# Performance work log

Measured on AMD Instinct MI355X. Metric: run time of the kernel, lower is better.

## Reference

```python
import jax, jax.numpy as jnp
import numpy as np

C = 256
GROUPS = 32
EPS = 1e-5


def setup_inputs() -> dict:
    key = jax.random.key(0)
    ks = jax.random.split(key, 6)
    b, c, H, W = 8, C, 64, 64
    s = 1.0 / np.sqrt(c)
    return {
        "x": jax.random.normal(ks[0], (b, c, H, W), dtype=jnp.float32),
        "gn_scale": jnp.ones((c,), jnp.float32),
        "gn_bias": jnp.zeros((c,), jnp.float32),
        "wq": jax.random.normal(ks[1], (c, c), jnp.float32) * s,
        "bq": jnp.zeros((c,), jnp.float32),
        "wk": jax.random.normal(ks[2], (c, c), jnp.float32) * s,
        "bk": jnp.zeros((c,), jnp.float32),
        "wv": jax.random.normal(ks[3], (c, c), jnp.float32) * s,
        "bv": jnp.zeros((c,), jnp.float32),
        "wo": jax.random.normal(ks[4], (c, c), jnp.float32) * s,
        "bo": jnp.zeros((c,), jnp.float32),
    }


def reference(x, gn_scale, gn_bias, wq, bq, wk, bk, wv, bv, wo, bo):
    b, c, H, W = x.shape
    N = H * W
    # GroupNorm(32, c)
    xg = x.reshape(b, GROUPS, c // GROUPS, H, W)
    mean = xg.mean(axis=(2, 3, 4), keepdims=True)
    var = xg.var(axis=(2, 3, 4), keepdims=True)
    xn = ((xg - mean) * jax.lax.rsqrt(var + EPS)).reshape(b, c, H, W)
    xn = xn * gn_scale[None, :, None, None] + gn_bias[None, :, None, None]
    xf = xn.reshape(b, c, N)  # [b, c, N]
    # 1x1 convs == per-pixel channel matmuls
    q = jnp.einsum('oc,bcn->bon', wq, xf) + bq[None, :, None]
    k = jnp.einsum('oc,bcn->bon', wk, xf) + bk[None, :, None]
    v = jnp.einsum('oc,bcn->bon', wv, xf) + bv[None, :, None]
    # attention: scores [b, N, N]
    scale = 1.0 / jnp.sqrt(jnp.asarray(c, x.dtype))
    w = jnp.einsum('bcn,bcm->bnm', q, k) * scale
    w = jax.nn.softmax(w, axis=-1)
    attn = jnp.einsum('bnm,bcm->bcn', w, v)  # [b, c, N]
    out = jnp.einsum('oc,bcn->bon', wo, attn) + bo[None, :, None]
    return x + out.reshape(b, c, H, W)
```

## Files before the change

kernel.cpp:

```cpp
#include <hip/hip_runtime.h>

typedef __attribute__((ext_vector_type(8))) short short8;
typedef __attribute__((ext_vector_type(4))) float floatx4;
typedef __attribute__((ext_vector_type(16))) float floatx16;
typedef __attribute__((ext_vector_type(4))) int intx4;

#define NPIX 4096
#define CH 256

static __device__ __forceinline__ unsigned short f2bf(float f) {
  union { float f; unsigned int u; } v; v.f = f;
  unsigned int u = v.u;
  return (unsigned short)((u + 0x7FFFu + ((u >> 16) & 1u)) >> 16);
}

static __device__ __forceinline__ unsigned int pk2bf(float a, float b) {
  union { float f; unsigned int u; } x, y; x.f = a; y.f = b;
  return __builtin_amdgcn_perm(y.u + 0x8000u, x.u + 0x8000u, 0x07060302u);
}

typedef __attribute__((address_space(3))) unsigned int lds_uint;
typedef const __attribute__((address_space(1))) unsigned int glob_uint;
static __device__ __forceinline__ void gload16(const void* g, void* l) {
  __builtin_amdgcn_global_load_lds((glob_uint*)g, (lds_uint*)l, 16, 0, 0);
}

__global__ void conv_weights_kernel(const float* __restrict__ wq, const float* __restrict__ wk,
                                    const float* __restrict__ wv, const float* __restrict__ wo,
                                    unsigned short* __restrict__ wqkv, unsigned short* __restrict__ wob) {
  int i = blockIdx.x * 256 + threadIdx.x;
  wqkv[i]          = f2bf(wq[i]);
  wqkv[65536 + i]  = f2bf(wk[i]);
  wqkv[131072 + i] = f2bf(wv[i]);
  wob[i]           = f2bf(wo[i]);
}

__global__ __launch_bounds__(256) void gn_kernel(const float* __restrict__ x,
                                                 const float* __restrict__ gsc,
                                                 const float* __restrict__ gbi,
                                                 unsigned short* __restrict__ xnT) {
  int blk = blockIdx.x; int b = blk >> 5; int g = blk & 31;
  int c0 = g * 8;
  const float* xb = x + ((size_t)b * CH + c0) * NPIX;
  int tid = threadIdx.x;
  float s = 0.f, ss = 0.f;
#pragma unroll
  for (int ci = 0; ci < 8; ++ci) {
    const floatx4* p = (const floatx4*)(xb + (size_t)ci * NPIX);
    for (int n4 = tid; n4 < 1024; n4 += 256) {
      floatx4 v = p[n4];
      s += v[0] + v[1] + v[2] + v[3];
      ss += v[0]*v[0] + v[1]*v[1] + v[2]*v[2] + v[3]*v[3];
    }
  }
#pragma unroll
  for (int o = 32; o > 0; o >>= 1) { s += __shfl_down(s, o); ss += __shfl_down(ss, o); }
  __shared__ float red[10];
  int wid = tid >> 6;
  if ((tid & 63) == 0) { red[wid] = s; red[4 + wid] = ss; }
  __syncthreads();
  if (tid == 0) {
    float S = red[0] + red[1] + red[2] + red[3];
    float SS = red[4] + red[5] + red[6] + red[7];
    float mean = S * (1.f / 32768.f);
    float var = SS * (1.f / 32768.f) - mean * mean;
    red[8] = mean; red[9] = rsqrtf(var + 1e-5f);
  }
  __syncthreads();
  float mean = red[8], rstd = red[9];
  float sc[8], bi[8];
#pragma unroll
  for (int ci = 0; ci < 8; ++ci) {
    float scale = gsc[c0 + ci] * rstd;
    sc[ci] = scale;
    bi[ci] = gbi[c0 + ci] - mean * scale;
  }
  for (int n4 = tid; n4 < 1024; n4 += 256) {
    floatx4 v[8];
#pragma unroll
    for (int ci = 0; ci < 8; ++ci) v[ci] = ((const floatx4*)(xb + (size_t)ci * NPIX))[n4];
#pragma unroll
    for (int j = 0; j < 4; ++j) {
      alignas(16) unsigned short tmp[8];
#pragma unroll
      for (int ci = 0; ci < 8; ++ci) tmp[ci] = f2bf(v[ci][j] * sc[ci] + bi[ci]);
      *(intx4*)(xnT + ((size_t)(b * NPIX + n4 * 4 + j)) * CH + c0) = *(const intx4*)tmp;
    }
  }
}

__global__ __launch_bounds__(256, 2) void qkv_gemm(
    const unsigned short* __restrict__ wqkv, const unsigned short* __restrict__ xnT,
    const float* __restrict__ bq, const float* __restrict__ bk, const float* __restrict__ bv,
    unsigned short* __restrict__ qT, unsigned short* __restrict__ kT, unsigned short* __restrict__ vC) {
  int nt = blockIdx.x, ot = blockIdx.y, bz = blockIdx.z;
  int which = bz % 3, b = bz / 3;
  const unsigned short* W = wqkv + which * 65536;
  const float* bias = which == 0 ? bq : (which == 1 ? bk : bv);
  const unsigned short* X = xnT + (size_t)b * NPIX * CH;
  int o0 = ot * 128, n0 = nt * 128;

  __shared__ unsigned short As[128 * 64];
  __shared__ unsigned short Bs[128 * 64];

  int tid = threadIdx.x;
  int wave = tid >> 6, lane = tid & 63, quad = lane >> 4, l16 = lane & 15;
  int wm = (wave >> 1) * 64, wn = (wave & 1) * 64;

  floatx4 acc[4][4];
#pragma unroll
  for (int i = 0; i < 4; ++i)
#pragma unroll
    for (int j = 0; j < 4; ++j) acc[i][j] = (floatx4){0.f, 0.f, 0.f, 0.f};

  for (int k0 = 0; k0 < 256; k0 += 64) {
    __syncthreads();
#pragma unroll
    for (int c2 = 0; c2 < 4; ++c2) {
      int row = wave * 32 + c2 * 8 + (lane >> 3);
      int sc = (lane & 7) ^ (row & 7);
      gload16(W + (size_t)(o0 + row) * CH + k0 + sc * 8, &As[(wave * 32 + c2 * 8) * 64]);
      gload16(X + (size_t)(n0 + row) * CH + k0 + sc * 8, &Bs[(wave * 32 + c2 * 8) * 64]);
    }
    __syncthreads();
#pragma unroll
    for (int s = 0; s < 2; ++s) {
      short8 af[4], bf[4];
#pragma unroll
      for (int i = 0; i < 4; ++i) {
        int m = wm + i * 16 + l16;
        af[i] = *(const short8*)(As + m * 64 + (((s * 4 + quad) ^ (m & 7)) * 8));
        int n = wn + i * 16 + l16;
        bf[i] = *(const short8*)(Bs + n * 64 + (((s * 4 + quad) ^ (n & 7)) * 8));
      }
#pragma unroll
      for (int i = 0; i < 4; ++i)
#pragma unroll
        for (int j = 0; j < 4; ++j)
          acc[i][j] = __builtin_amdgcn_mfma_f32_16x16x32_bf16(af[i], bf[j], acc[i][j], 0, 0, 0);
    }
  }

  if (which < 2) {
    float qs = (which == 0) ? 0.090168440f : 1.0f;
    unsigned short* outp = (which == 0 ? qT : kT) + (size_t)b * NPIX * CH;
#pragma unroll
    for (int i = 0; i < 4; ++i) {
      int obase = o0 + wm + i * 16 + quad * 4;
      float bias4[4];
#pragma unroll
      for (int r = 0; r < 4; ++r) bias4[r] = bias[obase + r];
#pragma unroll
      for (int j = 0; j < 4; ++j) {
        int n = n0 + wn + j * 16 + l16;
        uint2 pk;
        pk.x = pk2bf((acc[i][j][0] + bias4[0]) * qs, (acc[i][j][1] + bias4[1]) * qs);
        pk.y = pk2bf((acc[i][j][2] + bias4[2]) * qs, (acc[i][j][3] + bias4[3]) * qs);
        *(uint2*)(outp + (size_t)n * CH + obase) = pk;
      }
    }
  } else {
    unsigned short* outp = vC + (size_t)b * CH * NPIX;
#pragma unroll
    for (int i = 0; i < 4; ++i)
#pragma unroll
      for (int r = 0; r < 4; ++r) {
        int o = o0 + wm + i * 16 + quad * 4 + r;
        float bb = bias[o];
#pragma unroll
        for (int j = 0; j < 4; ++j) {
          int n = n0 + wn + j * 16 + l16;
          outp[(size_t)o * NPIX + n] = f2bf(acc[i][j][r] + bb);
        }
      }
  }
}

__global__ __launch_bounds__(512, 2) void attn_kernel(
    const unsigned short* __restrict__ qT, const unsigned short* __restrict__ kT,
    const unsigned short* __restrict__ vC, unsigned short* __restrict__ aT) {
  __shared__ unsigned short Klds[2][64 * 256];
  __shared__ unsigned short Vlds[2][256 * 64];
  __shared__ unsigned short Plds[128 * 64];
  __shared__ float lred[128][2];

  const int tid = threadIdx.x;
  const int w = tid >> 6, lane = tid & 63;
  const int l32 = lane & 31, h = lane >> 5;
  const int b = blockIdx.x & 7, qt = blockIdx.x >> 3;
  const int qbase = qt * 128;

  const unsigned short* Kb = kT + (size_t)b * NPIX * CH;
  const unsigned short* Vb = vC + (size_t)b * CH * NPIX;

  const int msl = (w & 1) * 32, qsl = (w >> 1) * 32;
  const int csl = (w & 3) * 64, qh = (w >> 2) * 64;

  short8 qf[16];
  {
    const unsigned short* qp = qT + ((size_t)(b * NPIX + qbase + qsl + l32)) * CH + h * 8;
#pragma unroll
    for (int s = 0; s < 16; ++s) qf[s] = *(const short8*)(qp + s * 16);
  }

  floatx16 oacc[2][2] = {};
  float l_acc = 0.f;

#define STAGE(KT)                                                                         \
  {                                                                                       \
    int m0_ = (KT) * 64;                                                                  \
    int bb_ = (KT) & 1;                                                                   \
    if (w < 4) {                                                                          \
      _Pragma("unroll") for (int j = 0; j < 8; ++j) {                                     \
        int r0 = w * 16 + j * 2 + (lane >> 5);                                            \
        gload16(Kb + (size_t)(m0_ + r0) * CH + (((lane & 31) ^ (r0 & 7)) * 8),            \
                &Klds[bb_][(w * 16 + j * 2) * 256]);                                      \
      }                                                                                   \
    } else {                                                                              \
      _Pragma("unroll") for (int j = 0; j < 8; ++j) {                                     \
        int c_ = (w - 4) * 64 + j * 8 + (lane >> 3);                                      \
        gload16(Vb + (size_t)c_ * NPIX + m0_ + (((lane & 7) ^ (c_ & 7)) * 8),             \
                &Vlds[bb_][((w - 4) * 64 + j * 8) * 64]);                                 \
      }                                                                                   \
    }                                                                                     \
  }

  STAGE(0);

  for (int kt = 0; kt < 64; ++kt) {
    const int buf = kt & 1;
    asm volatile("s_waitcnt vmcnt(0) lgkmcnt(0)\ns_barrier" ::: "memory");
    if (kt + 1 < 64) STAGE(kt + 1);

    floatx16 sacc = {};
    {
      const int m = msl + l32;
      const unsigned short* kr = &Klds[buf][m * 256];
      const int mx = m & 7;
#pragma unroll
      for (int s = 0; s < 16; ++s) {
        short8 kf = *(const short8*)(kr + (((s * 2 + h) ^ mx) * 8));
        sacc = __builtin_amdgcn_mfma_f32_32x32x16_bf16(kf, qf[s], sacc, 0, 0, 0);
      }
    }
    float sum = 0.f;
#pragma unroll
    for (int r = 0; r < 16; ++r) {
      float p = exp2f(sacc[r]);
      sacc[r] = p; sum += p;
    }
    sum += __shfl_xor(sum, 32);
    l_acc += sum;

    {
      int qrow = qsl + l32;
#pragma unroll
      for (int t = 0; t < 4; ++t) {
        int phys = ((msl >> 3) + t) ^ (qrow & 7);
        uint2 wv;
        wv.x = pk2bf(sacc[4 * t], sacc[4 * t + 1]);
        wv.y = pk2bf(sacc[4 * t + 2], sacc[4 * t + 3]);
        *(uint2*)&Plds[qrow * 64 + phys * 8 + h * 4] = wv;
      }
    }
    asm volatile("s_waitcnt lgkmcnt(0)\ns_barrier" ::: "memory");

#pragma unroll
    for (int mstep = 0; mstep < 4; ++mstep) {
      short8 pf[2], vf[2];
#pragma unroll
      for (int qsub = 0; qsub < 2; ++qsub) {
        int q = qh + qsub * 32 + l32;
        pf[qsub] = *(const short8*)&Plds[q * 64 + (((mstep * 2 + h) ^ (q & 7)) * 8)];
      }
#pragma unroll
      for (int csub = 0; csub < 2; ++csub) {
        int c = csl + csub * 32 + l32;
        vf[csub] = *(const short8*)&Vlds[buf][c * 64 + (((mstep * 2 + h) ^ (c & 7)) * 8)];
      }
#pragma unroll
      for (int csub = 0; csub < 2; ++csub)
#pragma unroll
        for (int qsub = 0; qsub < 2; ++qsub)
          oacc[csub][qsub] =
              __builtin_amdgcn_mfma_f32_32x32x16_bf16(vf[csub], pf[qsub], oacc[csub][qsub], 0, 0, 0);
    }
  }
#undef STAGE

  if (lane < 32) lred[qsl + l32][w & 1] = l_acc;
  __syncthreads();
  float inv[2];
#pragma unroll
  for (int qsub = 0; qsub < 2; ++qsub) {
    int q = qh + qsub * 32 + l32;
    inv[qsub] = 1.f / (lred[q][0] + lred[q][1]);
  }
  unsigned short* ab = aT + (size_t)b * NPIX * CH;
#pragma unroll
  for (int csub = 0; csub < 2; ++csub)
#pragma unroll
    for (int qsub = 0; qsub < 2; ++qsub) {
      int qg = qbase + qh + qsub * 32 + l32;
      float iv = inv[qsub];
#pragma unroll
      for (int t = 0; t < 4; ++t) {
        int c = csl + csub * 32 + 8 * t + 4 * h;
        uint2 wv;
        wv.x = pk2bf(oacc[csub][qsub][4 * t] * iv, oacc[csub][qsub][4 * t + 1] * iv);
        wv.y = pk2bf(oacc[csub][qsub][4 * t + 2] * iv, oacc[csub][qsub][4 * t + 3] * iv);
        *(uint2*)(ab + (size_t)qg * CH + c) = wv;
      }
    }
}

__global__ __launch_bounds__(256, 2) void out_gemm(
    const unsigned short* __restrict__ wob, const unsigned short* __restrict__ aT,
    const float* __restrict__ bo, const float* __restrict__ x, float* __restrict__ outp) {
  int nt = blockIdx.x, ot = blockIdx.y, b = blockIdx.z;
  const unsigned short* A = aT + (size_t)b * NPIX * CH;
  int o0 = ot * 128, n0 = nt * 128;

  __shared__ unsigned short As[128 * 64];
  __shared__ unsigned short Bs[128 * 64];

  int tid = threadIdx.x;
  int wave = tid >> 6, lane = tid & 63, quad = lane >> 4, l16 = lane & 15;
  int wm = (wave >> 1) * 64, wn = (wave & 1) * 64;

  floatx4 acc[4][4];
#pragma unroll
  for (int i = 0; i < 4; ++i)
#pragma unroll
    for (int j = 0; j < 4; ++j) acc[i][j] = (floatx4){0.f, 0.f, 0.f, 0.f};

  for (int k0 = 0; k0 < 256; k0 += 64) {
    __syncthreads();
#pragma unroll
    for (int c2 = 0; c2 < 4; ++c2) {
      int row = wave * 32 + c2 * 8 + (lane >> 3);
      int sc = (lane & 7) ^ (row & 7);
      gload16(wob + (size_t)(o0 + row) * CH + k0 + sc * 8, &As[(wave * 32 + c2 * 8) * 64]);
      gload16(A + (size_t)(n0 + row) * CH + k0 + sc * 8, &Bs[(wave * 32 + c2 * 8) * 64]);
    }
    __syncthreads();
#pragma unroll
    for (int s = 0; s < 2; ++s) {
      short8 af[4], bf[4];
#pragma unroll
      for (int i = 0; i < 4; ++i) {
        int m = wm + i * 16 + l16;
        af[i] = *(const short8*)(As + m * 64 + (((s * 4 + quad) ^ (m & 7)) * 8));
        int n = wn + i * 16 + l16;
        bf[i] = *(const short8*)(Bs + n * 64 + (((s * 4 + quad) ^ (n & 7)) * 8));
      }
#pragma unroll
      for (int i = 0; i < 4; ++i)
#pragma unroll
        for (int j = 0; j < 4; ++j)
          acc[i][j] = __builtin_amdgcn_mfma_f32_16x16x32_bf16(af[i], bf[j], acc[i][j], 0, 0, 0);
    }
  }

#pragma unroll
  for (int i = 0; i < 4; ++i)
#pragma unroll
    for (int r = 0; r < 4; ++r) {
      int o = o0 + wm + i * 16 + quad * 4 + r;
      float bb = bo[o];
#pragma unroll
      for (int j = 0; j < 4; ++j) {
        int n = n0 + wn + j * 16 + l16;
        size_t idx = ((size_t)b * CH + o) * NPIX + n;
        outp[idx] = x[idx] + bb + acc[i][j][r];
      }
    }
}

extern "C" void kernel_launch(void* const* d_in, const int* in_sizes, int n_in,
                              void* d_out, int out_size, void* d_ws, size_t ws_size,
                              hipStream_t stream) {
  const float* x   = (const float*)d_in[0];
  const float* gsc = (const float*)d_in[1];
  const float* gbi = (const float*)d_in[2];
  const float* wq  = (const float*)d_in[3];
  const float* bq  = (const float*)d_in[4];
  const float* wk  = (const float*)d_in[5];
  const float* bk  = (const float*)d_in[6];
  const float* wv  = (const float*)d_in[7];
  const float* bv  = (const float*)d_in[8];
  const float* wo  = (const float*)d_in[9];
  const float* bo  = (const float*)d_in[10];
  float* out = (float*)d_out;

  char* ws = (char*)d_ws;
  unsigned short* xnT  = (unsigned short*)(ws);
  unsigned short* qT   = (unsigned short*)(ws + 16777216);
  unsigned short* kT   = (unsigned short*)(ws + 33554432);
  unsigned short* vC   = (unsigned short*)(ws + 50331648);
  unsigned short* wqkv = (unsigned short*)(ws + 67108864);
  unsigned short* wob  = (unsigned short*)(ws + 67502080);
  unsigned short* aT   = (unsigned short*)(ws + 67633152);

  conv_weights_kernel<<<256, 256, 0, stream>>>(wq, wk, wv, wo, wqkv, wob);
  gn_kernel<<<256, 256, 0, stream>>>(x, gsc, gbi, xnT);
  dim3 g1(32, 2, 24);
  qkv_gemm<<<g1, 256, 0, stream>>>(wqkv, xnT, bq, bk, bv, qT, kT, vC);
  attn_kernel<<<256, 512, 0, stream>>>(qT, kT, vC, aT);
  dim3 g3(32, 2, 8);
  out_gemm<<<g3, 256, 0, stream>>>(wob, aT, bo, x, out);
}
```

Baseline: 320.9 us.

## Warp-specialize attention into score and PV waves; cache GroupNorm input in LDS

The attention kernel is split by role. Four waves compute QK^T scores and exp into double-buffered P tiles. The other four waves issue the K/V global-to-LDS loads and run the PV MFMAs one step behind, so score and output work overlap. The KV tile shrinks from 64 to 32 rows, which cuts LDS use (possibly allowing two blocks per CU) but doubles the number of barriers. Separately, the GroupNorm kernel keeps the group's input in 128KB of LDS so the normalization pass does not read x from global memory a second time, at the cost of occupancy for that kernel.

```diff
diff --git a/kernel.cpp b/kernel.cpp
--- a/kernel.cpp
+++ b/kernel.cpp
@@ -39,6 +39,8 @@
                                                  const float* __restrict__ gsc,
                                                  const float* __restrict__ gbi,
                                                  unsigned short* __restrict__ xnT) {
+  __shared__ float xs[8 * 4096];
+  __shared__ float red[12];
   int blk = blockIdx.x; int b = blk >> 5; int g = blk & 31;
   int c0 = g * 8;
   const float* xb = x + ((size_t)b * CH + c0) * NPIX;
@@ -47,15 +49,16 @@
 #pragma unroll
   for (int ci = 0; ci < 8; ++ci) {
     const floatx4* p = (const floatx4*)(xb + (size_t)ci * NPIX);
+    floatx4* ls = (floatx4*)(xs + ci * 4096);
     for (int n4 = tid; n4 < 1024; n4 += 256) {
       floatx4 v = p[n4];
+      ls[n4] = v;
       s += v[0] + v[1] + v[2] + v[3];
       ss += v[0]*v[0] + v[1]*v[1] + v[2]*v[2] + v[3]*v[3];
     }
   }
 #pragma unroll
   for (int o = 32; o > 0; o >>= 1) { s += __shfl_down(s, o); ss += __shfl_down(ss, o); }
-  __shared__ float red[10];
   int wid = tid >> 6;
   if ((tid & 63) == 0) { red[wid] = s; red[4 + wid] = ss; }
   __syncthreads();
@@ -78,7 +81,7 @@
   for (int n4 = tid; n4 < 1024; n4 += 256) {
     floatx4 v[8];
 #pragma unroll
-    for (int ci = 0; ci < 8; ++ci) v[ci] = ((const floatx4*)(xb + (size_t)ci * NPIX))[n4];
+    for (int ci = 0; ci < 8; ++ci) v[ci] = ((const floatx4*)(xs + ci * 4096))[n4];
 #pragma unroll
     for (int j = 0; j < 4; ++j) {
       alignas(16) unsigned short tmp[8];
@@ -179,10 +182,10 @@
 __global__ __launch_bounds__(512, 2) void attn_kernel(
     const unsigned short* __restrict__ qT, const unsigned short* __restrict__ kT,
     const unsigned short* __restrict__ vC, unsigned short* __restrict__ aT) {
-  __shared__ unsigned short Klds[2][64 * 256];
-  __shared__ unsigned short Vlds[2][256 * 64];
-  __shared__ unsigned short Plds[128 * 64];
-  __shared__ float lred[128][2];
+  __shared__ unsigned short Klds[2][32 * 256];
+  __shared__ unsigned short Vlds[2][256 * 32];
+  __shared__ unsigned short Plds[2][128 * 32];
+  __shared__ float lred[128];
 
   const int tid = threadIdx.x;
   const int w = tid >> 6, lane = tid & 63;
@@ -193,125 +196,133 @@
   const unsigned short* Kb = kT + (size_t)b * NPIX * CH;
   const unsigned short* Vb = vC + (size_t)b * CH * NPIX;
 
-  const int msl = (w & 1) * 32, qsl = (w >> 1) * 32;
-  const int csl = (w & 3) * 64, qh = (w >> 2) * 64;
-
-  short8 qf[16];
-  {
-    const unsigned short* qp = qT + ((size_t)(b * NPIX + qbase + qsl + l32)) * CH + h * 8;
-#pragma unroll
-    for (int s = 0; s < 16; ++s) qf[s] = *(const short8*)(qp + s * 16);
-  }
-
-  floatx16 oacc[2][2] = {};
-  float l_acc = 0.f;
-
-#define STAGE(KT)                                                                         \
-  {                                                                                       \
-    int m0_ = (KT) * 64;                                                                  \
-    int bb_ = (KT) & 1;                                                                   \
-    if (w < 4) {                                                                          \
-      _Pragma("unroll") for (int j = 0; j < 8; ++j) {                                     \
-        int r0 = w * 16 + j * 2 + (lane >> 5);                                            \
-        gload16(Kb + (size_t)(m0_ + r0) * CH + (((lane & 31) ^ (r0 & 7)) * 8),            \
-                &Klds[bb_][(w * 16 + j * 2) * 256]);                                      \
-      }                                                                                   \
-    } else {                                                                              \
-      _Pragma("unroll") for (int j = 0; j < 8; ++j) {                                     \
-        int c_ = (w - 4) * 64 + j * 8 + (lane >> 3);                                      \
-        gload16(Vb + (size_t)c_ * NPIX + m0_ + (((lane & 7) ^ (c_ & 7)) * 8),             \
-                &Vlds[bb_][((w - 4) * 64 + j * 8) * 64]);                                 \
-      }                                                                                   \
-    }                                                                                     \
-  }
-
-  STAGE(0);
-
-  for (int kt = 0; kt < 64; ++kt) {
-    const int buf = kt & 1;
-    asm volatile("s_waitcnt vmcnt(0) lgkmcnt(0)\ns_barrier" ::: "memory");
-    if (kt + 1 < 64) STAGE(kt + 1);
-
-    floatx16 sacc = {};
+#define BARRIER() asm volatile("s_waitcnt vmcnt(0) lgkmcnt(0)\ns_barrier" ::: "memory")
+
+  if (w < 4) {
+    const int qsl = w * 32;
+    const int q = qsl + l32;
+    const int swq = (q >> 1) & 3;
+    const int mx = l32 & 7;
+    short8 qf[16];
     {
-      const int m = msl + l32;
-      const unsigned short* kr = &Klds[buf][m * 256];
-      const int mx = m & 7;
-#pragma unroll
-      for (int s = 0; s < 16; ++s) {
-        short8 kf = *(const short8*)(kr + (((s * 2 + h) ^ mx) * 8));
-        sacc = __builtin_amdgcn_mfma_f32_32x32x16_bf16(kf, qf[s], sacc, 0, 0, 0);
-      }
-    }
-    float sum = 0.f;
-#pragma unroll
-    for (int r = 0; r < 16; ++r) {
-      float p = exp2f(sacc[r]);
-      sacc[r] = p; sum += p;
-    }
-    sum += __shfl_xor(sum, 32);
-    l_acc += sum;
-
-    {
-      int qrow = qsl + l32;
-#pragma unroll
-      for (int t = 0; t < 4; ++t) {
-        int phys = ((msl >> 3) + t) ^ (qrow & 7);
-        uint2 wv;
-        wv.x = pk2bf(sacc[4 * t], sacc[4 * t + 1]);
-        wv.y = pk2bf(sacc[4 * t + 2], sacc[4 * t + 3]);
-        *(uint2*)&Plds[qrow * 64 + phys * 8 + h * 4] = wv;
-      }
-    }
-    asm volatile("s_waitcnt lgkmcnt(0)\ns_barrier" ::: "memory");
-
-#pragma unroll
-    for (int mstep = 0; mstep < 4; ++mstep) {
-      short8 pf[2], vf[2];
-#pragma unroll
-      for (int qsub = 0; qsub < 2; ++qsub) {
-        int q = qh + qsub * 32 + l32;
-        pf[qsub] = *(const short8*)&Plds[q * 64 + (((mstep * 2 + h) ^ (q & 7)) * 8)];
-      }
-#pragma unroll
-      for (int csub = 0; csub < 2; ++csub) {
-        int c = csl + csub * 32 + l32;
-        vf[csub] = *(const short8*)&Vlds[buf][c * 64 + (((mstep * 2 + h) ^ (c & 7)) * 8)];
-      }
-#pragma unroll
-      for (int csub = 0; csub < 2; ++csub)
-#pragma unroll
-        for (int qsub = 0; qsub < 2; ++qsub)
-          oacc[csub][qsub] =
-              __builtin_amdgcn_mfma_f32_32x32x16_bf16(vf[csub], pf[qsub], oacc[csub][qsub], 0, 0, 0);
-    }
-  }
-#undef STAGE
-
-  if (lane < 32) lred[qsl + l32][w & 1] = l_acc;
-  __syncthreads();
-  float inv[2];
-#pragma unroll
-  for (int qsub = 0; qsub < 2; ++qsub) {
-    int q = qh + qsub * 32 + l32;
-    inv[qsub] = 1.f / (lred[q][0] + lred[q][1]);
-  }
-  unsigned short* ab = aT + (size_t)b * NPIX * CH;
-#pragma unroll
-  for (int csub = 0; csub < 2; ++csub)
-#pragma unroll
-    for (int qsub = 0; qsub < 2; ++qsub) {
-      int qg = qbase + qh + qsub * 32 + l32;
-      float iv = inv[qsub];
-#pragma unroll
-      for (int t = 0; t < 4; ++t) {
-        int c = csl + csub * 32 + 8 * t + 4 * h;
-        uint2 wv;
-        wv.x = pk2bf(oacc[csub][qsub][4 * t] * iv, oacc[csub][qsub][4 * t + 1] * iv);
-        wv.y = pk2bf(oacc[csub][qsub][4 * t + 2] * iv, oacc[csub][qsub][4 * t + 3] * iv);
-        *(uint2*)(ab + (size_t)qg * CH + c) = wv;
-      }
-    }
+      const unsigned short* qp = qT + ((size_t)(b * NPIX + qbase + q)) * CH + h * 8;
+#pragma unroll
+      for (int s = 0; s < 16; ++s) qf[s] = *(const short8*)(qp + s * 16);
+    }
+    float l_acc = 0.f;
+    for (int t = 0; t < 129; ++t) {
+      BARRIER();
+      if (t < 128) {
+        const unsigned short* kr = &Klds[t & 1][l32 * 256];
+        floatx16 s0 = {}, s1 = {};
+#pragma unroll
+        for (int s = 0; s < 8; ++s) {
+          short8 kf0 = *(const short8*)(kr + (((s * 2 + h) ^ mx) * 8));
+          short8 kf1 = *(const short8*)(kr + ((((s + 8) * 2 + h) ^ mx) * 8));
+          s0 = __builtin_amdgcn_mfma_f32_32x32x16_bf16(kf0, qf[s], s0, 0, 0, 0);
+          s1 = __builtin_amdgcn_mfma_f32_32x32x16_bf16(kf1, qf[s + 8], s1, 0, 0, 0);
+        }
+        float sum = 0.f;
+#pragma unroll
+        for (int r = 0; r < 16; ++r) {
+          float pv = exp2f(s0[r] + s1[r]);
+          s0[r] = pv; sum += pv;
+        }
+        l_acc += sum;
+        unsigned short* Pw = Plds[t & 1];
+#pragma unroll
+        for (int t4 = 0; t4 < 4; ++t4) {
+          int phys = t4 ^ swq;
+          uint2 wv;
+          wv.x = pk2bf(s0[4 * t4], s0[4 * t4 + 1]);
+          wv.y = pk2bf(s0[4 * t4 + 2], s0[4 * t4 + 3]);
+          *(uint2*)&Pw[q * 32 + phys * 8 + h * 4] = wv;
+        }
+      }
+    }
+    l_acc += __shfl_xor(l_acc, 32);
+    if (lane < 32) lred[q] = l_acc;
+    BARRIER();
+  } else {
+    const int p = w - 4;
+    const int csl = p * 64;
+    floatx16 oacc[2][4];
+#pragma unroll
+    for (int i = 0; i < 2; ++i)
+#pragma unroll
+      for (int j = 0; j < 4; ++j) oacc[i][j] = (floatx16){0.f};
+#pragma unroll
+    for (int j = 0; j < 4; ++j) {
+      int r0 = p * 8 + j * 2 + h;
+      gload16(Kb + (size_t)r0 * CH + (((lane & 31) ^ (r0 & 7)) * 8),
+              &Klds[0][(p * 8 + j * 2) * 256]);
+    }
+    for (int t = 0; t < 129; ++t) {
+      BARRIER();
+      if (t < 128) {
+        const int m0 = t * 32;
+#pragma unroll
+        for (int j = 0; j < 4; ++j) {
+          int r = p * 64 + j * 16 + (lane >> 2);
+          gload16(Vb + (size_t)r * NPIX + m0 + (((lane & 3) ^ ((r >> 1) & 3)) * 8),
+                  &Vlds[t & 1][(p * 64 + j * 16) * 32]);
+        }
+        if (t + 1 < 128) {
+          const int m1 = (t + 1) * 32;
+#pragma unroll
+          for (int j = 0; j < 4; ++j) {
+            int r0 = p * 8 + j * 2 + h;
+            gload16(Kb + (size_t)(m1 + r0) * CH + (((lane & 31) ^ (r0 & 7)) * 8),
+                    &Klds[(t + 1) & 1][(p * 8 + j * 2) * 256]);
+          }
+        }
+      }
+      if (t >= 1) {
+        const int pb = (t - 1) & 1;
+#pragma unroll
+        for (int mstep = 0; mstep < 2; ++mstep) {
+          short8 pf[4], vf[2];
+#pragma unroll
+          for (int qs = 0; qs < 4; ++qs) {
+            int q = qs * 32 + l32;
+            pf[qs] = *(const short8*)&Plds[pb][q * 32 + (((mstep * 2 + h) ^ ((q >> 1) & 3)) * 8)];
+          }
+#pragma unroll
+          for (int cs = 0; cs < 2; ++cs) {
+            int c = csl + cs * 32 + l32;
+            vf[cs] = *(const short8*)&Vlds[pb][c * 32 + (((mstep * 2 + h) ^ ((c >> 1) & 3)) * 8)];
+          }
+#pragma unroll
+          for (int cs = 0; cs < 2; ++cs)
+#pragma unroll
+            for (int qs = 0; qs < 4; ++qs)
+              oacc[cs][qs] =
+                  __builtin_amdgcn_mfma_f32_32x32x16_bf16(vf[cs], pf[qs], oacc[cs][qs], 0, 0, 0);
+        }
+      }
+    }
+    BARRIER();
+    float iv[4];
+#pragma unroll
+    for (int qs = 0; qs < 4; ++qs) iv[qs] = 1.f / lred[qs * 32 + l32];
+    unsigned short* ab = aT + (size_t)b * NPIX * CH;
+#pragma unroll
+    for (int cs = 0; cs < 2; ++cs)
+#pragma unroll
+      for (int qs = 0; qs < 4; ++qs) {
+        size_t qg = qbase + qs * 32 + l32;
+        float v = iv[qs];
+#pragma unroll
+        for (int t4 = 0; t4 < 4; ++t4) {
+          int c = csl + cs * 32 + 8 * t4 + 4 * h;
+          uint2 wv;
+          wv.x = pk2bf(oacc[cs][qs][4 * t4] * v, oacc[cs][qs][4 * t4 + 1] * v);
+          wv.y = pk2bf(oacc[cs][qs][4 * t4 + 2] * v, oacc[cs][qs][4 * t4 + 3] * v);
+          *(uint2*)(ab + qg * CH + c) = wv;
+        }
+      }
+  }
+#undef BARRIER
 }
 
 __global__ __launch_bounds__(256, 2) void out_gemm(
```

Measured after the change: 346.5 us. +8.0%, slower.
